# Kernel optimization log

Measured on AMD Instinct MI355X. Metric: run time of the kernel, lower is better.

The kernel has to match this reference:

```python
import jax, jax.numpy as jnp
import numpy as np

EPS = 1e-12
H = 256
W = 256
RANK = 4
CTX = 1024
BATCH = 32
FF = (H + W) * RANK * 4  # 8192
STD = 0.001


def _norm(x, axis):
    # torch: (x - mean) / sqrt(var(unbiased) + eps)
    m = jnp.mean(x, axis=axis, keepdims=True)
    v = jnp.var(x, axis=axis, keepdims=True, ddof=1)
    return (x - m) / jnp.sqrt(v + EPS)


def _norm_polar(x):
    # x: [B, N, 2]; magnitude-normalize relative to per-batch max magnitude
    x_abs = jnp.sqrt(x[..., 0] ** 2 + x[..., 1] ** 2 + EPS)          # [B, N]
    h = x_abs / (jnp.max(x_abs, axis=-1, keepdims=True) + EPS)       # [B, N]
    xn = x / (x_abs[..., None] + EPS)                                # [B, N, 2]
    return jnp.stack([h * xn[..., 0], h * xn[..., 1]], axis=-1)


def setup_inputs() -> dict:
    key = jax.random.key(0)
    ks = jax.random.split(key, 12)

    def lin(k, fan_in, shape):
        b = 1.0 / np.sqrt(fan_in)
        return jax.random.uniform(k, shape, jnp.float32, -b, b)

    weights_static = jnp.concatenate([
        jax.random.normal(ks[9], (1, H, W, 2), jnp.float32) * STD,
        jax.random.normal(ks[10], (1, H, W, 2), jnp.float32) * STD
        + jnp.array([1.0, 0.0], jnp.float32),
    ], axis=0)  # [2, H, W, 2]

    return {
        "x": jax.random.normal(ks[0], (BATCH, CTX), jnp.float32),
        "W_in": lin(ks[1], CTX, (FF, CTX)),
        "b_in": lin(ks[2], CTX, (FF,)),
        "W_gate": lin(ks[3], CTX, (FF, CTX)),
        "b_gate": lin(ks[4], CTX, (FF,)),
        "W_t": lin(ks[5], FF, (FF, FF)),
        "b_t": lin(ks[6], FF, (FF,)),
        "conv_w": lin(ks[7], RANK, (RANK, RANK)),  # 1x1 conv kernel [out, in]
        "conv_b": lin(ks[8], RANK, (RANK,)),
        "weights_static": weights_static,
        "weights_mod": jax.random.normal(ks[11], (4, H, W), jnp.float32) * STD,
    }


def reference(x, W_in, b_in, W_gate, b_gate, W_t, b_t, conv_w, conv_b,
              weights_static, weights_mod):
    b = x.shape[0]
    # dual linear projections (dropout p=0 -> identity)
    xt = x @ W_in.T + b_in            # [B, FF]
    xg = x @ W_gate.T + b_gate        # [B, FF]
    stack = jnp.stack([xt, xg], axis=0).reshape(2, b, 4, -1)
    stack = _norm(stack, -1)
    ctx = (stack[0] * jnp.tanh(stack[1])).reshape(b, -1)   # gated, [B, FF]
    ctx = ctx @ W_t.T + b_t                                 # [B, FF]
    ctx = ctx.reshape(b, 4, RANK, H + W)
    modc = _norm(ctx, -1)
    # outer product -> [B, 4, RANK, H, W]
    mod = jnp.tanh(jnp.einsum('bkri,bkrj->bkrij', modc[..., :H], modc[..., H:]))
    # channel 0: 1x1 conv over rank channels, then sum channels (keepdim)
    mod_real = jnp.einsum('oi,bihw->bohw', conv_w, mod[:, 0]) + conv_b[None, :, None, None]
    mod_real = jnp.sum(mod_real, axis=1, keepdims=True)     # [B, 1, H, W]
    mod_other = jnp.sum(mod[:, 1:], axis=2)                 # [B, 3, H, W]
    mod = jnp.concatenate([mod_real, mod_other], axis=1)    # [B, 4, H, W]
    mod = weights_mod[None] * mod

    A0 = weights_static[0]            # [H, W, 2]
    A1 = weights_static[1]            # [H, W, 2]
    Bm = jnp.moveaxis(mod[:, 0:2], 1, -1)                   # [B, H, W, 2]
    ms_r = A1[..., 0] * Bm[..., 0] - A1[..., 1] * Bm[..., 1]
    ms_i = A1[..., 0] * Bm[..., 1] - A1[..., 1] * Bm[..., 0]
    mod_scaled = jnp.stack([ms_r, ms_i], axis=-1)           # [B, H, W, 2]
    mod_scaled = _norm_polar(mod_scaled.reshape(b, H * W, 2)).reshape(b, H, W, 2)

    mag = jnp.sqrt(mod_scaled[..., 0] ** 2 + mod_scaled[..., 1] ** 2 + EPS)
    mag = jnp.sqrt(jnp.mean(mag, axis=(-1, -2)) + EPS)      # [B]
    mod_scaled = mod_scaled / mag[:, None, None, None]

    mod_weights = A0[None] + mod_scaled                     # [B, H, W, 2]

    mod_proj = jnp.moveaxis(mod[:, 2:], 1, -1)              # [B, H, W, 2]
    mod_proj = _norm_polar(mod_proj.reshape(b, H * W, 2)).reshape(b, H, W, 2)
    den = jnp.sqrt(mod_proj[..., 0] ** 2 + mod_proj[..., 1] ** 2 + EPS)
    theta_cos = mod_proj[..., 0] / den
    theta_sin = mod_proj[..., 1] / den
    weights = mod_weights[..., 0] * theta_cos + mod_weights[..., 1] * theta_sin
    return weights  # [B, H, W]
```

## Files before the change

kernel.cpp:

```cpp
#include <hip/hip_runtime.h>
#include <cstddef>

#define NB   32
#define CTXD 1024
#define FFD  8192
#define HD   256
#define WD   256
#define NPIX 65536
#define EPSF 1e-12f

typedef __attribute__((ext_vector_type(8))) short bf16x8;
typedef __attribute__((ext_vector_type(4))) float f32x4;


__device__ __forceinline__ float ftanh(float x){
  float ax = fabsf(x);
  float e  = __expf(2.0f*ax);
  float r  = 1.0f - 2.0f*__builtin_amdgcn_rcpf(e + 1.0f);
  return copysignf(r, x);
}

__device__ __forceinline__ unsigned short f2bf(float f){
  unsigned u = __float_as_uint(f);
  unsigned r = (u + 0x7FFFu + ((u >> 16) & 1u)) >> 16;
  return (unsigned short)r;
}
__device__ __forceinline__ float bf2f(unsigned short s){
  return __uint_as_float((unsigned)s << 16);
}

__device__ __forceinline__ void split3(float f, unsigned short& s0,
                                       unsigned short& s1, unsigned short& s2){
  s0 = f2bf(f);
  float r1 = f - bf2f(s0);
  s1 = f2bf(r1);
  float r2 = r1 - bf2f(s1);
  s2 = f2bf(r2);
}

__device__ __forceinline__ void gload_lds16(const float* g, float* l){
  __builtin_amdgcn_global_load_lds(
      (__attribute__((address_space(1))) void*)const_cast<float*>(g),
      (__attribute__((address_space(3))) void*)l, 16, 0, 0);
}

__device__ __forceinline__ void block_reduce4(float& a, float& b, float& c, float& d){
  for (int off = 32; off > 0; off >>= 1){
    a += __shfl_down(a, off); b += __shfl_down(b, off);
    c += __shfl_down(c, off); d += __shfl_down(d, off);
  }
  __shared__ float lds[16];
  int wid = threadIdx.x >> 6, lane = threadIdx.x & 63;
  if (lane == 0){ lds[wid*4+0]=a; lds[wid*4+1]=b; lds[wid*4+2]=c; lds[wid*4+3]=d; }
  __syncthreads();
  a = (lds[0]+lds[4])+(lds[8]+lds[12]);
  b = (lds[1]+lds[5])+(lds[9]+lds[13]);
  c = (lds[2]+lds[6])+(lds[10]+lds[14]);
  d = (lds[3]+lds[7])+(lds[11]+lds[15]);
}

__device__ __forceinline__ void pixel_core(
    const float* __restrict__ lds, int h, int w, int pix,
    float cw0, float cw1, float cw2, float cw3, float cb,
    const float* __restrict__ wmod, const float* __restrict__ wstat,
    float& r_, float& i_, float& p_, float& q_){
  float sk[4];
  #pragma unroll
  for (int k = 0; k < 4; ++k){
    float acc = 0.f;
    #pragma unroll
    for (int r = 0; r < 4; ++r){
      int kr = k*4 + r;
      float u  = lds[kr*512 + h];
      float vv = lds[kr*512 + 256 + w];
      float tt = ftanh(u*vv);
      float cwr = (r==0)?cw0:(r==1)?cw1:(r==2)?cw2:cw3;
      acc += (k==0) ? cwr*tt : tt;
    }
    sk[k] = acc;
  }
  sk[0] += cb;
  float m0 = sk[0]*wmod[0*NPIX+pix];
  float m1 = sk[1]*wmod[1*NPIX+pix];
  float m2 = sk[2]*wmod[2*NPIX+pix];
  float m3 = sk[3]*wmod[3*NPIX+pix];
  float2 A1 = *(const float2*)(wstat + (size_t)(NPIX + pix)*2);
  r_ = A1.x*m0 - A1.y*m1;
  i_ = A1.x*m1 - A1.y*m0;
  p_ = m2; q_ = m3;
}


__global__ __launch_bounds__(256) void k_prep(
    const float* __restrict__ x, unsigned short* __restrict__ P,
    float* __restrict__ red){
  int g = blockIdx.x*256 + threadIdx.x;
  if (g < 64) red[g] = 0.0f;
  int b = g >> 7, grp = g & 127;
  int koff = grp*8;
  int c = grp >> 2, kg = grp & 3;
  const float* src = x + (size_t)b*CTXD + koff;
  float4 v0 = *(const float4*)(src), v1 = *(const float4*)(src+4);
  float vv[8] = {v0.x,v0.y,v0.z,v0.w,v1.x,v1.y,v1.z,v1.w};
  bf16x8 a0, a1, a2;
  #pragma unroll
  for (int e = 0; e < 8; ++e){
    unsigned short s0,s1,s2; split3(vv[e],s0,s1,s2);
    a0[e]=(short)s0; a1[e]=(short)s1; a2[e]=(short)s2;
  }
  size_t base = (size_t)c*3072 + (b>>4)*512 + kg*128 + (b&15)*8;
  *(bf16x8*)(P + base)        = a0;
  *(bf16x8*)(P + base + 1024) = a1;
  *(bf16x8*)(P + base + 2048) = a2;
}

template<int KC>
__global__ __launch_bounds__(256) void k_gemm_mfma(
    const float* __restrict__ W0, const float* __restrict__ W1,
    const unsigned short* __restrict__ BP,
    float* __restrict__ Cp, int K, size_t zstride){
  const float* __restrict__ W = blockIdx.z ? W1 : W0;
  int wave = threadIdx.x >> 6;
  int lane = threadIdx.x & 63;
  int f0   = blockIdx.x*64 + wave*16;
  int kc   = blockIdx.y;
  int row  = lane & 15;
  int kg   = lane >> 4;
  int rot  = blockIdx.x & (KC-1);
  const float* Wb = W + (size_t)(f0+row)*K + kc*KC*32 + kg*8;
  const unsigned short* Bb = BP + (size_t)kc*KC*3072 + kg*128 + row*8;
  f32x4 acc0={0.f,0.f,0.f,0.f}, acc1={0.f,0.f,0.f,0.f};
  const float* wp = Wb + rot*32;
  float4 w0 = *(const float4*)(wp), w1 = *(const float4*)(wp+4);
  for (int c = 0; c < KC; ++c){
    int rc = (c + rot) & (KC-1);
    const unsigned short* bp = Bb + (size_t)rc*3072;
    bf16x8 b0h0 = *(const bf16x8*)(bp);
    bf16x8 b0h1 = *(const bf16x8*)(bp +  512);
    bf16x8 b1h0 = *(const bf16x8*)(bp + 1024);
    bf16x8 b1h1 = *(const bf16x8*)(bp + 1536);
    bf16x8 b2h0 = *(const bf16x8*)(bp + 2048);
    bf16x8 b2h1 = *(const bf16x8*)(bp + 2560);
    float4 cw0 = w0, cw1 = w1;
    if (c + 1 < KC){
      int rn = (c + 1 + rot) & (KC-1);
      wp = Wb + rn*32;
      w0 = *(const float4*)(wp); w1 = *(const float4*)(wp+4);
    }
    bf16x8 a0, a1, a2;
    float wv[8] = {cw0.x,cw0.y,cw0.z,cw0.w,cw1.x,cw1.y,cw1.z,cw1.w};
    #pragma unroll
    for (int e = 0; e < 8; ++e){
      unsigned short s0,s1,s2; split3(wv[e],s0,s1,s2);
      a0[e]=(short)s0; a1[e]=(short)s1; a2[e]=(short)s2;
    }
    acc0 = __builtin_amdgcn_mfma_f32_16x16x32_bf16(a0, b0h0, acc0, 0,0,0);
    acc1 = __builtin_amdgcn_mfma_f32_16x16x32_bf16(a0, b0h1, acc1, 0,0,0);
    acc0 = __builtin_amdgcn_mfma_f32_16x16x32_bf16(a0, b1h0, acc0, 0,0,0);
    acc1 = __builtin_amdgcn_mfma_f32_16x16x32_bf16(a0, b1h1, acc1, 0,0,0);
    acc0 = __builtin_amdgcn_mfma_f32_16x16x32_bf16(a1, b0h0, acc0, 0,0,0);
    acc1 = __builtin_amdgcn_mfma_f32_16x16x32_bf16(a1, b0h1, acc1, 0,0,0);
    acc0 = __builtin_amdgcn_mfma_f32_16x16x32_bf16(a0, b2h0, acc0, 0,0,0);
    acc1 = __builtin_amdgcn_mfma_f32_16x16x32_bf16(a0, b2h1, acc1, 0,0,0);
    acc0 = __builtin_amdgcn_mfma_f32_16x16x32_bf16(a1, b1h0, acc0, 0,0,0);
    acc1 = __builtin_amdgcn_mfma_f32_16x16x32_bf16(a1, b1h1, acc1, 0,0,0);
    acc0 = __builtin_amdgcn_mfma_f32_16x16x32_bf16(a2, b0h0, acc0, 0,0,0);
    acc1 = __builtin_amdgcn_mfma_f32_16x16x32_bf16(a2, b0h1, acc1, 0,0,0);
  }
  float* __restrict__ C = Cp + (size_t)blockIdx.z*zstride + (size_t)kc*(FFD*32);
  #pragma unroll
  for (int r = 0; r < 4; ++r){
    int f = f0 + kg*4 + r;
    C[(size_t)f*32 + row]      = acc0[r];
    C[(size_t)f*32 + 16 + row] = acc1[r];
  }
}

template<int STEPS>
__global__ __launch_bounds__(256) void k_gemm_lds(
    const float* __restrict__ W, const unsigned short* __restrict__ BP,
    float* __restrict__ Cp, int K){
  __shared__ float tile[2][4096];
  const int t    = threadIdx.x;
  const int wv   = t >> 6, lane = t & 63;
  const int f0   = blockIdx.x * 64;
  const int kc   = blockIdx.y;
  const int row  = lane & 15, kg = lane >> 4;
  const int srot = blockIdx.x & (STEPS - 1);
  const size_t kslice = (size_t)kc * STEPS * 64;

  f32x4 acc0 = {0.f,0.f,0.f,0.f}, acc1 = {0.f,0.f,0.f,0.f};

  auto stage = [&](int buf, int s){
    const size_t kbase = kslice + (size_t)s*64;
    #pragma unroll
    for (int i = 0; i < 4; ++i){
      int r = wv*16 + i*4 + (lane >> 4);
      const float* gsrc = W + (size_t)(f0 + r)*K + kbase + (lane & 15)*4;
      gload_lds16(gsrc, &tile[buf][(wv*16 + i*4)*64]);
    }
  };

  int cur = 0;
  stage(0, srot);
  __syncthreads();

  for (int s = 0; s < STEPS; ++s){
    const int sc = (s + srot) & (STEPS - 1);
    const int k0 = kc*STEPS*2 + sc*2;
    const unsigned short* bp0 = BP + (size_t)k0*3072     + kg*128 + row*8;
    const unsigned short* bp1 = BP + (size_t)(k0+1)*3072 + kg*128 + row*8;
    bf16x8 c0b0h0 = *(const bf16x8*)(bp0);
    bf16x8 c0b0h1 = *(const bf16x8*)(bp0 +  512);
    bf16x8 c0b1h0 = *(const bf16x8*)(bp0 + 1024);
    bf16x8 c0b1h1 = *(const bf16x8*)(bp0 + 1536);
    bf16x8 c0b2h0 = *(const bf16x8*)(bp0 + 2048);
    bf16x8 c0b2h1 = *(const bf16x8*)(bp0 + 2560);
    bf16x8 c1b0h0 = *(const bf16x8*)(bp1);
    bf16x8 c1b0h1 = *(const bf16x8*)(bp1 +  512);
    bf16x8 c1b1h0 = *(const bf16x8*)(bp1 + 1024);
    bf16x8 c1b1h1 = *(const bf16x8*)(bp1 + 1536);
    bf16x8 c1b2h0 = *(const bf16x8*)(bp1 + 2048);
    bf16x8 c1b2h1 = *(const bf16x8*)(bp1 + 2560);
    if (s + 1 < STEPS) stage(cur ^ 1, (s + 1 + srot) & (STEPS - 1));
    #pragma unroll
    for (int c = 0; c < 2; ++c){
      const float* wp = &tile[cur][(wv*16 + row)*64 + c*32 + kg*8];
      float4 w0 = *(const float4*)(wp);
      float4 w1 = *(const float4*)(wp + 4);
      bf16x8 a0, a1, a2;
      float wv8[8] = {w0.x,w0.y,w0.z,w0.w,w1.x,w1.y,w1.z,w1.w};
      #pragma unroll
      for (int e = 0; e < 8; ++e){
        unsigned short s0,s1,s2; split3(wv8[e],s0,s1,s2);
        a0[e]=(short)s0; a1[e]=(short)s1; a2[e]=(short)s2;
      }
      bf16x8 b0h0 = c ? c1b0h0 : c0b0h0, b0h1 = c ? c1b0h1 : c0b0h1;
      bf16x8 b1h0 = c ? c1b1h0 : c0b1h0, b1h1 = c ? c1b1h1 : c0b1h1;
      bf16x8 b2h0 = c ? c1b2h0 : c0b2h0, b2h1 = c ? c1b2h1 : c0b2h1;
      acc0 = __builtin_amdgcn_mfma_f32_16x16x32_bf16(a0, b0h0, acc0, 0,0,0);
      acc1 = __builtin_amdgcn_mfma_f32_16x16x32_bf16(a0, b0h1, acc1, 0,0,0);
      acc0 = __builtin_amdgcn_mfma_f32_16x16x32_bf16(a0, b1h0, acc0, 0,0,0);
      acc1 = __builtin_amdgcn_mfma_f32_16x16x32_bf16(a0, b1h1, acc1, 0,0,0);
      acc0 = __builtin_amdgcn_mfma_f32_16x16x32_bf16(a1, b0h0, acc0, 0,0,0);
      acc1 = __builtin_amdgcn_mfma_f32_16x16x32_bf16(a1, b0h1, acc1, 0,0,0);
      acc0 = __builtin_amdgcn_mfma_f32_16x16x32_bf16(a0, b2h0, acc0, 0,0,0);
      acc1 = __builtin_amdgcn_mfma_f32_16x16x32_bf16(a0, b2h1, acc1, 0,0,0);
      acc0 = __builtin_amdgcn_mfma_f32_16x16x32_bf16(a1, b1h0, acc0, 0,0,0);
      acc1 = __builtin_amdgcn_mfma_f32_16x16x32_bf16(a1, b1h1, acc1, 0,0,0);
      acc0 = __builtin_amdgcn_mfma_f32_16x16x32_bf16(a2, b0h0, acc0, 0,0,0);
      acc1 = __builtin_amdgcn_mfma_f32_16x16x32_bf16(a2, b0h1, acc1, 0,0,0);
    }
    __syncthreads();
    cur ^= 1;
  }

  float* __restrict__ C = Cp + (size_t)kc*(FFD*32);
  #pragma unroll
  for (int r = 0; r < 4; ++r){
    int f = f0 + wv*16 + kg*4 + r;
    C[(size_t)f*32 + row]      = acc0[r];
    C[(size_t)f*32 + 16 + row] = acc1[r];
  }
}

__global__ __launch_bounds__(256) void k_reduce1(
    const float* __restrict__ Cp, const float* __restrict__ bin,
    const float* __restrict__ bg, float* __restrict__ xtT,
    float* __restrict__ xgT){
  int g = blockIdx.x*256 + threadIdx.x;
  int m = g >> 18, idx = g & 262143;
  int f = idx >> 5;
  const float* __restrict__ cp = Cp + (size_t)m*(8ull*FFD*32);
  float s = (m ? bg : bin)[f];
  #pragma unroll
  for (int sI = 0; sI < 8; ++sI) s += cp[(size_t)sI*(FFD*32) + idx];
  (m ? xgT : xtT)[idx] = s;
}

__global__ __launch_bounds__(256) void k_reduce2(
    const float* __restrict__ Cp, const float* __restrict__ bias,
    float* __restrict__ outT){
  int g = blockIdx.x*256 + threadIdx.x;
  int f = g >> 5;
  float s = bias[f];
  #pragma unroll
  for (int sI = 0; sI < 16; ++sI) s += Cp[(size_t)sI*(FFD*32) + g];
  outT[g] = s;
}

__global__ __launch_bounds__(256) void k_normgate(
    const float* __restrict__ xtT, const float* __restrict__ xgT,
    unsigned short* __restrict__ P){
  int b = blockIdx.x >> 2, g4 = blockIdx.x & 3;
  int t = threadIdx.x;
  int f8 = g4*2048 + t*8;
  float vt[8], vg[8];
  float st=0.f, sst=0.f, sg=0.f, ssg=0.f;
  #pragma unroll
  for (int i = 0; i < 8; ++i){
    int f = f8 + i;
    float a = xtT[(size_t)f*NB + b];
    float c = xgT[(size_t)f*NB + b];
    vt[i]=a; vg[i]=c;
    st += a; sst += a*a; sg += c; ssg += c*c;
  }
  block_reduce4(st, sst, sg, ssg);
  float mt = st * (1.0f/2048.0f);
  float it = rsqrtf((sst - st*mt) * (1.0f/2047.0f) + EPSF);
  float mg = sg * (1.0f/2048.0f);
  float ig = rsqrtf((ssg - sg*mg) * (1.0f/2047.0f) + EPSF);
  bf16x8 a0, a1, a2;
  #pragma unroll
  for (int i = 0; i < 8; ++i){
    float nt = (vt[i]-mt)*it;
    float ng = (vg[i]-mg)*ig;
    float cv = nt * ftanh(ng);
    unsigned short s0,s1,s2; split3(cv,s0,s1,s2);
    a0[i]=(short)s0; a1[i]=(short)s1; a2[i]=(short)s2;
  }
  int c2 = f8 >> 5, kg = (f8 >> 3) & 3;
  size_t base = (size_t)c2*3072 + (b>>4)*512 + kg*128 + (b&15)*8;
  *(bf16x8*)(P + base)        = a0;
  *(bf16x8*)(P + base + 1024) = a1;
  *(bf16x8*)(P + base + 2048) = a2;
}

__global__ __launch_bounds__(256) void k_norm512(
    const float* __restrict__ ctx2T, float* __restrict__ modc){
  int b = blockIdx.x >> 4, kr = blockIdx.x & 15;
  int t = threadIdx.x;
  int base = kr*512;
  float v0 = ctx2T[(base + t      )*NB + b];
  float v1 = ctx2T[(base + 256 + t)*NB + b];
  float s = v0+v1, ss = v0*v0 + v1*v1, d0=0.f, d1=0.f;
  block_reduce4(s, ss, d0, d1);
  float m   = s * (1.0f/512.0f);
  float inv = rsqrtf((ss - s*m) * (1.0f/511.0f) + EPSF);
  modc[b*FFD + base + t      ] = (v0-m)*inv;
  modc[b*FFD + base + 256 + t] = (v1-m)*inv;
}

__global__ __launch_bounds__(256) void k_scan(
    const float* __restrict__ modc,
    const float* __restrict__ convw, const float* __restrict__ convb,
    const float* __restrict__ wmod, const float* __restrict__ wstat,
    float* __restrict__ red, float* __restrict__ magpart){
  int b = blockIdx.x >> 4, chunk = blockIdx.x & 15;
  int t = threadIdx.x;
  __shared__ float lds[16*512];
  #pragma unroll
  for (int i = 0; i < 8; ++i){
    float4 v = *(const float4*)(modc + (size_t)b*FFD + (i*256 + t)*4);
    *(float4*)(lds + (i*256 + t)*4) = v;
  }
  float cw0 = convw[0]+convw[4]+convw[8]+convw[12];
  float cw1 = convw[1]+convw[5]+convw[9]+convw[13];
  float cw2 = convw[2]+convw[6]+convw[10]+convw[14];
  float cw3 = convw[3]+convw[7]+convw[11]+convw[15];
  float cb  = convb[0]+convb[1]+convb[2]+convb[3];
  __syncthreads();
  int w = t;
  float mxs = 0.f, mxp = 0.f, sas = 0.f;
  for (int it = 0; it < 16; ++it){
    int h = chunk*16 + it;
    int pix = h*WD + w;
    float r_, i_, p_, q_;
    pixel_core(lds, h, w, pix, cw0, cw1, cw2, cw3, cb, wmod, wstat,
               r_, i_, p_, q_);
    float as = sqrtf(r_*r_ + i_*i_ + EPSF);
    float ap = sqrtf(p_*p_ + q_*q_ + EPSF);
    mxs = fmaxf(mxs, as); mxp = fmaxf(mxp, ap);
    sas += as;
  }
  for (int off = 32; off > 0; off >>= 1){
    mxs = fmaxf(mxs, __shfl_down(mxs, off));
    mxp = fmaxf(mxp, __shfl_down(mxp, off));
    sas += __shfl_down(sas, off);
  }
  __shared__ float lred[12];
  int wid = t >> 6, lane = t & 63;
  if (lane == 0){ lred[wid] = mxs; lred[4+wid] = mxp; lred[8+wid] = sas; }
  __syncthreads();
  if (t == 0){
    float a = fmaxf(fmaxf(lred[0],lred[1]), fmaxf(lred[2],lred[3]));
    float p = fmaxf(fmaxf(lred[4],lred[5]), fmaxf(lred[6],lred[7]));
    float s = (lred[8]+lred[9])+(lred[10]+lred[11]);
    atomicMax((int*)&red[b],    __float_as_int(a));
    atomicMax((int*)&red[32+b], __float_as_int(p));
    magpart[b*16 + chunk] = s;
  }
}

__global__ __launch_bounds__(256) void k_final(
    const float* __restrict__ modc,
    const float* __restrict__ convw, const float* __restrict__ convb,
    const float* __restrict__ wmod, const float* __restrict__ wstat,
    const float* __restrict__ red, const float* __restrict__ magpart,
    float* __restrict__ out){
  int b = blockIdx.x >> 4, chunk = blockIdx.x & 15;
  int t = threadIdx.x;
  __shared__ float lds[16*512];
  __shared__ float s_im;
  if (t < 16){
    float v = magpart[b*16 + t];
    for (int off = 8; off > 0; off >>= 1) v += __shfl_down(v, off);
    if (t == 0){
      float maxs = red[b];
      s_im = rsqrtf(v*(1.0f/65536.0f)/(maxs + EPSF) + EPSF);
    }
  }
  #pragma unroll
  for (int i = 0; i < 8; ++i){
    float4 v = *(const float4*)(modc + (size_t)b*FFD + (i*256 + t)*4);
    *(float4*)(lds + (i*256 + t)*4) = v;
  }
  float cw0 = convw[0]+convw[4]+convw[8]+convw[12];
  float cw1 = convw[1]+convw[5]+convw[9]+convw[13];
  float cw2 = convw[2]+convw[6]+convw[10]+convw[14];
  float cw3 = convw[3]+convw[7]+convw[11]+convw[15];
  float cb  = convb[0]+convb[1]+convb[2]+convb[3];
  __syncthreads();
  float im = s_im;
  float maxs = red[b], maxp = red[32+b];
  int w = t;
  for (int it = 0; it < 16; ++it){
    int h = chunk*16 + it;
    int pix = h*WD + w;
    float r_, i_, p_, q_;
    pixel_core(lds, h, w, pix, cw0, cw1, cw2, cw3, cb, wmod, wstat,
               r_, i_, p_, q_);
    float as = sqrtf(r_*r_ + i_*i_ + EPSF);
    float fs = (as/(maxs+EPSF))/(as+EPSF)*im;
    float2 A0 = *(const float2*)(wstat + (size_t)pix*2);
    float mwr = A0.x + fs*r_;
    float mwi = A0.y + fs*i_;
    float ap = sqrtf(p_*p_ + q_*q_ + EPSF);
    float fp = (ap/(maxp+EPSF))/(ap+EPSF);
    float mpr = fp*p_, mpi = fp*q_;
    float den = sqrtf(mpr*mpr + mpi*mpi + EPSF);
    out[(size_t)b*NPIX + pix] = (mwr*mpr + mwi*mpi)/den;
  }
}


extern "C" void kernel_launch(void* const* d_in, const int* in_sizes, int n_in,
                              void* d_out, int out_size, void* d_ws, size_t ws_size,
                              hipStream_t stream){
  const float* x     = (const float*)d_in[0];
  const float* Win   = (const float*)d_in[1];
  const float* bin   = (const float*)d_in[2];
  const float* Wg    = (const float*)d_in[3];
  const float* bg    = (const float*)d_in[4];
  const float* Wt    = (const float*)d_in[5];
  const float* bt    = (const float*)d_in[6];
  const float* convw = (const float*)d_in[7];
  const float* convb = (const float*)d_in[8];
  const float* wstat = (const float*)d_in[9];
  const float* wmod  = (const float*)d_in[10];
  float* out = (float*)d_out;
  float* ws  = (float*)d_ws;

  float* xtT   = ws;
  float* xgT   = ws + 262144;
  float* ctx2T = ws;
  float* modc  = ws + 262144;
  unsigned short* P2 = (unsigned short*)(ws + 524288);
  unsigned short* P1 = (unsigned short*)(ws + 917504);
  float* Cp    = ws + 966656;
  float* red     = ws + 5160960;
  float* magpart = ws + 5161024;

  k_prep<<<16, 256, 0, stream>>>(x, P1, red);
  k_gemm_mfma<4><<<dim3(128,8,2), 256, 0, stream>>>(Win, Wg, P1,
                                                    Cp, CTXD, 8ull*FFD*32);
  k_reduce1<<<2048, 256, 0, stream>>>(Cp, bin, bg, xtT, xgT);
  k_normgate<<<128, 256, 0, stream>>>(xtT, xgT, P2);
  k_gemm_lds<8><<<dim3(128,16), 256, 0, stream>>>(Wt, P2, Cp, FFD);
  k_reduce2<<<1024, 256, 0, stream>>>(Cp, bt, ctx2T);
  k_norm512<<<512, 256, 0, stream>>>(ctx2T, modc);
  k_scan<<<512, 256, 0, stream>>>(modc, convw, convb, wmod, wstat, red, magpart);
  k_final<<<512, 256, 0, stream>>>(modc, convw, convb, wmod, wstat, red,
                                   magpart, out);
}
```

Measured before the change: 163.5 us.

## Unify projection GEMMs on LDS path and drop block barriers for wave-local waits

The separate register-prefetch kernel for the two input projections is removed. Both projections now use the LDS double-buffered GEMM, with a z dimension choosing the weight matrix and the K split cut from 8 to 4, so the first reduction sums 4 partials. Each wave stages and reads only its own 16 rows, so the per-step __syncthreads is replaced by an explicit s_waitcnt vmcnt(4) plus a sched_barrier. Step rotation is also staggered per wave to spread DRAM access. This relies on the loads staying wave-local, and the hard-coded vmcnt count makes the code fragile if the number of outstanding loads changes.

```diff
diff --git a/kernel.cpp b/kernel.cpp
--- a/kernel.cpp
+++ b/kernel.cpp
@@ -114,97 +114,35 @@
   *(bf16x8*)(P + base + 2048) = a2;
 }
 
-template<int KC>
-__global__ __launch_bounds__(256) void k_gemm_mfma(
+template<int STEPS, int WROT>
+__global__ __launch_bounds__(256) void k_gemm_lds(
     const float* __restrict__ W0, const float* __restrict__ W1,
     const unsigned short* __restrict__ BP,
     float* __restrict__ Cp, int K, size_t zstride){
-  const float* __restrict__ W = blockIdx.z ? W1 : W0;
-  int wave = threadIdx.x >> 6;
-  int lane = threadIdx.x & 63;
-  int f0   = blockIdx.x*64 + wave*16;
-  int kc   = blockIdx.y;
-  int row  = lane & 15;
-  int kg   = lane >> 4;
-  int rot  = blockIdx.x & (KC-1);
-  const float* Wb = W + (size_t)(f0+row)*K + kc*KC*32 + kg*8;
-  const unsigned short* Bb = BP + (size_t)kc*KC*3072 + kg*128 + row*8;
-  f32x4 acc0={0.f,0.f,0.f,0.f}, acc1={0.f,0.f,0.f,0.f};
-  const float* wp = Wb + rot*32;
-  float4 w0 = *(const float4*)(wp), w1 = *(const float4*)(wp+4);
-  for (int c = 0; c < KC; ++c){
-    int rc = (c + rot) & (KC-1);
-    const unsigned short* bp = Bb + (size_t)rc*3072;
-    bf16x8 b0h0 = *(const bf16x8*)(bp);
-    bf16x8 b0h1 = *(const bf16x8*)(bp +  512);
-    bf16x8 b1h0 = *(const bf16x8*)(bp + 1024);
-    bf16x8 b1h1 = *(const bf16x8*)(bp + 1536);
-    bf16x8 b2h0 = *(const bf16x8*)(bp + 2048);
-    bf16x8 b2h1 = *(const bf16x8*)(bp + 2560);
-    float4 cw0 = w0, cw1 = w1;
-    if (c + 1 < KC){
-      int rn = (c + 1 + rot) & (KC-1);
-      wp = Wb + rn*32;
-      w0 = *(const float4*)(wp); w1 = *(const float4*)(wp+4);
-    }
-    bf16x8 a0, a1, a2;
-    float wv[8] = {cw0.x,cw0.y,cw0.z,cw0.w,cw1.x,cw1.y,cw1.z,cw1.w};
-    #pragma unroll
-    for (int e = 0; e < 8; ++e){
-      unsigned short s0,s1,s2; split3(wv[e],s0,s1,s2);
-      a0[e]=(short)s0; a1[e]=(short)s1; a2[e]=(short)s2;
-    }
-    acc0 = __builtin_amdgcn_mfma_f32_16x16x32_bf16(a0, b0h0, acc0, 0,0,0);
-    acc1 = __builtin_amdgcn_mfma_f32_16x16x32_bf16(a0, b0h1, acc1, 0,0,0);
-    acc0 = __builtin_amdgcn_mfma_f32_16x16x32_bf16(a0, b1h0, acc0, 0,0,0);
-    acc1 = __builtin_amdgcn_mfma_f32_16x16x32_bf16(a0, b1h1, acc1, 0,0,0);
-    acc0 = __builtin_amdgcn_mfma_f32_16x16x32_bf16(a1, b0h0, acc0, 0,0,0);
-    acc1 = __builtin_amdgcn_mfma_f32_16x16x32_bf16(a1, b0h1, acc1, 0,0,0);
-    acc0 = __builtin_amdgcn_mfma_f32_16x16x32_bf16(a0, b2h0, acc0, 0,0,0);
-    acc1 = __builtin_amdgcn_mfma_f32_16x16x32_bf16(a0, b2h1, acc1, 0,0,0);
-    acc0 = __builtin_amdgcn_mfma_f32_16x16x32_bf16(a1, b1h0, acc0, 0,0,0);
-    acc1 = __builtin_amdgcn_mfma_f32_16x16x32_bf16(a1, b1h1, acc1, 0,0,0);
-    acc0 = __builtin_amdgcn_mfma_f32_16x16x32_bf16(a2, b0h0, acc0, 0,0,0);
-    acc1 = __builtin_amdgcn_mfma_f32_16x16x32_bf16(a2, b0h1, acc1, 0,0,0);
-  }
-  float* __restrict__ C = Cp + (size_t)blockIdx.z*zstride + (size_t)kc*(FFD*32);
-  #pragma unroll
-  for (int r = 0; r < 4; ++r){
-    int f = f0 + kg*4 + r;
-    C[(size_t)f*32 + row]      = acc0[r];
-    C[(size_t)f*32 + 16 + row] = acc1[r];
-  }
-}
-
-template<int STEPS>
-__global__ __launch_bounds__(256) void k_gemm_lds(
-    const float* __restrict__ W, const unsigned short* __restrict__ BP,
-    float* __restrict__ Cp, int K){
   __shared__ float tile[2][4096];
   const int t    = threadIdx.x;
   const int wv   = t >> 6, lane = t & 63;
   const int f0   = blockIdx.x * 64;
   const int kc   = blockIdx.y;
   const int row  = lane & 15, kg = lane >> 4;
-  const int srot = blockIdx.x & (STEPS - 1);
+  const float* __restrict__ W = blockIdx.z ? W1 : W0;
+  const int srot = ((int)blockIdx.x + wv*WROT) & (STEPS - 1);
   const size_t kslice = (size_t)kc * STEPS * 64;
 
   f32x4 acc0 = {0.f,0.f,0.f,0.f}, acc1 = {0.f,0.f,0.f,0.f};
 
-  auto stage = [&](int buf, int s){
-    const size_t kbase = kslice + (size_t)s*64;
+  auto stage = [&](int buf, int sc){
+    const size_t kbase = kslice + (size_t)sc*64;
     #pragma unroll
     for (int i = 0; i < 4; ++i){
-      int r = wv*16 + i*4 + (lane >> 4);
-      const float* gsrc = W + (size_t)(f0 + r)*K + kbase + (lane & 15)*4;
+      int r = wv*16 + i*4 + kg;
+      const float* gsrc = W + (size_t)(f0 + r)*K + kbase + row*4;
       gload_lds16(gsrc, &tile[buf][(wv*16 + i*4)*64]);
     }
   };
 
   int cur = 0;
   stage(0, srot);
-  __syncthreads();
-
   for (int s = 0; s < STEPS; ++s){
     const int sc = (s + srot) & (STEPS - 1);
     const int k0 = kc*STEPS*2 + sc*2;
@@ -223,6 +161,8 @@
     bf16x8 c1b2h0 = *(const bf16x8*)(bp1 + 2048);
     bf16x8 c1b2h1 = *(const bf16x8*)(bp1 + 2560);
     if (s + 1 < STEPS) stage(cur ^ 1, (s + 1 + srot) & (STEPS - 1));
+    asm volatile("s_waitcnt vmcnt(4)" ::: "memory");
+    __builtin_amdgcn_sched_barrier(0);
     #pragma unroll
     for (int c = 0; c < 2; ++c){
       const float* wp = &tile[cur][(wv*16 + row)*64 + c*32 + kg*8];
@@ -251,11 +191,10 @@
       acc0 = __builtin_amdgcn_mfma_f32_16x16x32_bf16(a2, b0h0, acc0, 0,0,0);
       acc1 = __builtin_amdgcn_mfma_f32_16x16x32_bf16(a2, b0h1, acc1, 0,0,0);
     }
-    __syncthreads();
     cur ^= 1;
   }
 
-  float* __restrict__ C = Cp + (size_t)kc*(FFD*32);
+  float* __restrict__ C = Cp + (size_t)blockIdx.z*zstride + (size_t)kc*(FFD*32);
   #pragma unroll
   for (int r = 0; r < 4; ++r){
     int f = f0 + wv*16 + kg*4 + r;
@@ -271,10 +210,10 @@
   int g = blockIdx.x*256 + threadIdx.x;
   int m = g >> 18, idx = g & 262143;
   int f = idx >> 5;
-  const float* __restrict__ cp = Cp + (size_t)m*(8ull*FFD*32);
+  const float* __restrict__ cp = Cp + (size_t)m*(4ull*FFD*32);
   float s = (m ? bg : bin)[f];
   #pragma unroll
-  for (int sI = 0; sI < 8; ++sI) s += cp[(size_t)sI*(FFD*32) + idx];
+  for (int sI = 0; sI < 4; ++sI) s += cp[(size_t)sI*(FFD*32) + idx];
   (m ? xgT : xtT)[idx] = s;
 }
 
@@ -472,11 +411,12 @@
   float* magpart = ws + 5161024;
 
   k_prep<<<16, 256, 0, stream>>>(x, P1, red);
-  k_gemm_mfma<4><<<dim3(128,8,2), 256, 0, stream>>>(Win, Wg, P1,
-                                                    Cp, CTXD, 8ull*FFD*32);
+  k_gemm_lds<4,1><<<dim3(128,4,2), 256, 0, stream>>>(Win, Wg, P1,
+                                                     Cp, CTXD, 4ull*FFD*32);
   k_reduce1<<<2048, 256, 0, stream>>>(Cp, bin, bg, xtT, xgT);
   k_normgate<<<128, 256, 0, stream>>>(xtT, xgT, P2);
-  k_gemm_lds<8><<<dim3(128,16), 256, 0, stream>>>(Wt, P2, Cp, FFD);
+  k_gemm_lds<8,2><<<dim3(128,16,1), 256, 0, stream>>>(Wt, Wt, P2,
+                                                      Cp, FFD, 0);
   k_reduce2<<<1024, 256, 0, stream>>>(Cp, bt, ctx2T);
   k_norm512<<<512, 256, 0, stream>>>(ctx2T, modc);
   k_scan<<<512, 256, 0, stream>>>(modc, convw, convb, wmod, wstat, red, magpart);
```

New measurement: 163.9 us. About the same (+0.2%).
